# Kernel optimization log

Hardware: AMD Instinct MI355X
Metric: run time of the kernel (lower is better)

The kernel has to match this reference:

```python
import jax, jax.numpy as jnp
import numpy as np

B, S, D = 32, 1024, 512  # batch, seq_len, d_feat (= din = 2*dhid)

def setup_inputs() -> dict:
    key = jax.random.key(0)
    ks = jax.random.split(key, 8)
    x = jax.random.normal(ks[0], (B, S, D), dtype=jnp.float32)
    x_len = jax.random.randint(ks[1], (B,), 1, S + 1).astype(jnp.int32)
    w_score = jax.random.normal(ks[2], (D,), dtype=jnp.float32) * 0.02
    b_score = jnp.zeros((), dtype=jnp.float32)
    Wq = jax.random.normal(ks[3], (D, D), dtype=jnp.float32) * 0.02
    bq = jnp.zeros((D,), dtype=jnp.float32)
    Wk = jax.random.normal(ks[4], (D, D), dtype=jnp.float32) * 0.02
    bk = jnp.zeros((D,), dtype=jnp.float32)
    beta_raw = jax.random.uniform(ks[5], (1,), minval=-0.01, maxval=0.01, dtype=jnp.float32)
    return {"x": x, "x_len": x_len, "slot_idx": 0, "w_score": w_score, "b_score": b_score,
            "Wq": Wq, "bq": bq, "Wk": Wk, "bk": bk, "beta_raw": beta_raw}

def reference(x, x_len, slot_idx, w_score, b_score, Wq, bq, Wk, bk, beta_raw):
    # valid-position mask from per-sample lengths: [B, S]
    mask = jnp.arange(x.shape[1])[None, :] < x_len[:, None]
    neg_inf = jnp.float32(-jnp.inf)

    # ---- local branch: linear scorer -> masked softmax -> weighted sum ----
    local_scores = jnp.einsum('bsd,d->bs', x, w_score) + b_score          # [B, S]
    local_scores = jnp.where(mask, local_scores, neg_inf)
    local_w = jax.nn.softmax(local_scores, axis=1)
    c_local = jnp.einsum('bs,bsd->bd', local_w, x)                        # [B, D]

    # ---- global branch: QK bmm -> row-sum -> masked softmax -> weighted sum of x ----
    q = jnp.einsum('bsd,de->bse', x, Wq) + bq                             # [B, S, D]
    k = jnp.einsum('bsd,de->bse', x, Wk) + bk                             # [B, S, D]
    attn = jnp.einsum('bid,bjd->bij', q, k) / jnp.sqrt(jnp.float32(x.shape[2]))  # [B, S, S]
    g_scores = attn.sum(axis=2)                                           # [B, S] (sum over ALL j, as in source)
    g_scores = jnp.where(mask, g_scores, neg_inf)
    g_w = jax.nn.softmax(g_scores, axis=1)
    c_global = jnp.einsum('bs,bsd->bd', g_w, x)                           # [B, D]

    # ---- beta-weighted combination ----
    beta = jax.nn.sigmoid(beta_raw[slot_idx])
    c = c_local * beta + c_global * (1.0 - beta)
    return (x, c)
```

## Files before the change

kernel.cpp:

```cpp
#include <hip/hip_runtime.h>
#include <float.h>
#include <math.h>

#define BB 32
#define SS 1024
#define DD 512
#define NCH 32
#define CROWS 32
#define RW 8

typedef float f32x4 __attribute__((ext_vector_type(4)));

__device__ __forceinline__ float wave_reduce_add(float v) {
    #pragma unroll
    for (int m = 32; m >= 1; m >>= 1) v += __shfl_xor(v, m, 64);
    return v;
}

__global__ __launch_bounds__(256) void k_pass1(
    const float* __restrict__ x, const float* __restrict__ w_score,
    const int* __restrict__ x_len, float* __restrict__ out_x,
    float* __restrict__ xsum_part, float* __restrict__ lP,
    float* __restrict__ lm, float* __restrict__ lS)
{
    __shared__ float red_xsum[4][DD];
    __shared__ float red_ctx[4][DD];
    __shared__ float m_s[4], S_s[4];
    int b = blockIdx.x, sc = blockIdx.y;
    int wave = threadIdx.x >> 6, lane = threadIdx.x & 63, tid = threadIdx.x;
    int len = x_len[b];
    int s0 = sc * CROWS + wave * RW;
    size_t base = ((size_t)b * SS + s0) * DD;

    const f32x4* wr = (const f32x4*)w_score;
    f32x4 w0 = wr[lane], w1 = wr[lane + 64];

    f32x4 a[RW][2];
    #pragma unroll
    for (int r = 0; r < RW; ++r) {
        const f32x4* xr = (const f32x4*)(x + base + (size_t)r * DD);
        a[r][0] = xr[lane];
        a[r][1] = xr[lane + 64];
    }
    #pragma unroll
    for (int r = 0; r < RW; ++r) {
        f32x4* orow = (f32x4*)(out_x + base + (size_t)r * DD);
        __builtin_nontemporal_store(a[r][0], &orow[lane]);
        __builtin_nontemporal_store(a[r][1], &orow[lane + 64]);
    }
    float p[RW];
    f32x4 acc0 = {0,0,0,0}, acc1 = {0,0,0,0};
    #pragma unroll
    for (int r = 0; r < RW; ++r) {
        f32x4 t0 = a[r][0] * w0 + a[r][1] * w1;
        p[r] = t0.x + t0.y + t0.z + t0.w;
        acc0 += a[r][0];
        acc1 += a[r][1];
    }
    #pragma unroll
    for (int r = 0; r < RW; ++r) p[r] = wave_reduce_add(p[r]);
    float mw = -FLT_MAX;
    #pragma unroll
    for (int r = 0; r < RW; ++r) if (s0 + r < len) mw = fmaxf(mw, p[r]);
    float Sw = 0.f;
    f32x4 c0 = {0,0,0,0}, c1 = {0,0,0,0};
    #pragma unroll
    for (int r = 0; r < RW; ++r) {
        float wgt = (s0 + r < len) ? __expf(p[r] - mw) : 0.f;
        Sw += wgt;
        c0 += wgt * a[r][0];
        c1 += wgt * a[r][1];
    }
    f32x4* rx = (f32x4*)red_xsum[wave];
    f32x4* rc = (f32x4*)red_ctx[wave];
    rx[lane] = acc0; rx[lane + 64] = acc1;
    rc[lane] = c0;   rc[lane + 64] = c1;
    if (lane == 0) { m_s[wave] = mw; S_s[wave] = Sw; }
    __syncthreads();
    float mc = fmaxf(fmaxf(m_s[0], m_s[1]), fmaxf(m_s[2], m_s[3]));
    float e0 = __expf(m_s[0] - mc), e1 = __expf(m_s[1] - mc);
    float e2 = __expf(m_s[2] - mc), e3 = __expf(m_s[3] - mc);
    #pragma unroll
    for (int i = 0; i < 2; ++i) {
        int d = tid + i * 256;
        size_t off = ((size_t)b * NCH + sc) * DD + d;
        xsum_part[off] = red_xsum[0][d] + red_xsum[1][d] + red_xsum[2][d] + red_xsum[3][d];
        lP[off] = red_ctx[0][d]*e0 + red_ctx[1][d]*e1 + red_ctx[2][d]*e2 + red_ctx[3][d]*e3;
    }
    if (tid == 0) {
        lm[b * NCH + sc] = mc;
        lS[b * NCH + sc] = S_s[0]*e0 + S_s[1]*e1 + S_s[2]*e2 + S_s[3]*e3;
    }
}

__global__ __launch_bounds__(256) void k_ks(
    const float* __restrict__ xsum_part, const float* __restrict__ Wk,
    float* __restrict__ ks_part)
{
    __shared__ float xs[8][64];
    int dc = blockIdx.x, eb = blockIdx.y, bg = blockIdx.z;
    int tid = threadIdx.x;
    int e = eb * 256 + tid;
    #pragma unroll
    for (int k = 0; k < 2; ++k) {
        int i = tid + k * 256;
        int bi = i >> 6, dl = i & 63;
        int b = bg * 8 + bi, d = dc * 64 + dl;
        float v = 0.f;
        #pragma unroll 8
        for (int scc = 0; scc < NCH; ++scc)
            v += xsum_part[((size_t)b * NCH + scc) * DD + d];
        xs[bi][dl] = v;
    }
    __syncthreads();
    float acc[8] = {0,0,0,0,0,0,0,0};
    #pragma unroll 8
    for (int dl = 0; dl < 64; ++dl) {
        float w = Wk[(size_t)(dc * 64 + dl) * DD + e];
        #pragma unroll
        for (int bi = 0; bi < 8; ++bi) acc[bi] += xs[bi][dl] * w;
    }
    #pragma unroll
    for (int bi = 0; bi < 8; ++bi) {
        int b = bg * 8 + bi;
        ks_part[((size_t)dc * BB + b) * DD + e] = acc[bi];
    }
}

__global__ __launch_bounds__(256) void k_v(
    const float* __restrict__ ks_part, const float* __restrict__ Wq,
    const float* __restrict__ bk, float* __restrict__ v_part)
{
    __shared__ float wq_lds[256 * 65];
    __shared__ float ks_lds[8][64];
    int ec = blockIdx.x, db = blockIdx.y, bg = blockIdx.z;
    int tid = threadIdx.x;
    #pragma unroll
    for (int k = 0; k < 2; ++k) {
        int i = tid + k * 256;
        int bi = i >> 6, el = i & 63;
        int b = bg * 8 + bi, e = ec * 64 + el;
        float val = (float)SS * bk[e];
        #pragma unroll
        for (int dcc = 0; dcc < 8; ++dcc)
            val += ks_part[((size_t)dcc * BB + b) * DD + e];
        ks_lds[bi][el] = val;
    }
    #pragma unroll
    for (int it = 0; it < 16; ++it) {
        int idx = tid + it * 256;
        int rowd = idx >> 4, col4 = idx & 15;
        const f32x4 wv = *(const f32x4*)(Wq + (size_t)(db * 256 + rowd) * DD + ec * 64 + col4 * 4);
        float* dst = &wq_lds[rowd * 65 + col4 * 4];
        dst[0] = wv.x; dst[1] = wv.y; dst[2] = wv.z; dst[3] = wv.w;
    }
    __syncthreads();
    float acc[8] = {0,0,0,0,0,0,0,0};
    #pragma unroll 8
    for (int el = 0; el < 64; ++el) {
        float wq = wq_lds[tid * 65 + el];
        #pragma unroll
        for (int bi = 0; bi < 8; ++bi) acc[bi] += ks_lds[bi][el] * wq;
    }
    int d = db * 256 + tid;
    #pragma unroll
    for (int bi = 0; bi < 8; ++bi) {
        int b = bg * 8 + bi;
        v_part[((size_t)ec * BB + b) * DD + d] = acc[bi];
    }
}

__global__ __launch_bounds__(256) void k_pass2(
    const float* __restrict__ x, const float* __restrict__ v_part,
    const int* __restrict__ x_len,
    float* __restrict__ gP, float* __restrict__ gm, float* __restrict__ gS)
{
    __shared__ float v_lds[DD];
    __shared__ float red_ctx[4][DD];
    __shared__ float m_s[4], S_s[4];
    int b = blockIdx.x, sc = blockIdx.y;
    int wave = threadIdx.x >> 6, lane = threadIdx.x & 63, tid = threadIdx.x;
    int len = x_len[b];
    int s0 = sc * CROWS + wave * RW;
    size_t base = ((size_t)b * SS + s0) * DD;

    #pragma unroll
    for (int i = 0; i < 2; ++i) {
        int d = tid + i * 256;
        float vv = 0.f;
        #pragma unroll
        for (int ec = 0; ec < 8; ++ec) vv += v_part[((size_t)ec * BB + b) * DD + d];
        v_lds[d] = vv;
    }
    __syncthreads();
    const f32x4* vr = (const f32x4*)v_lds;
    f32x4 v0 = vr[lane], v1 = vr[lane + 64];

    f32x4 a[RW][2];
    #pragma unroll
    for (int r = 0; r < RW; ++r) {
        const f32x4* xr = (const f32x4*)(x + base + (size_t)r * DD);
        a[r][0] = xr[lane];
        a[r][1] = xr[lane + 64];
    }
    float p[RW];
    #pragma unroll
    for (int r = 0; r < RW; ++r) {
        f32x4 t0 = a[r][0] * v0 + a[r][1] * v1;
        p[r] = t0.x + t0.y + t0.z + t0.w;
    }
    #pragma unroll
    for (int r = 0; r < RW; ++r)
        p[r] = wave_reduce_add(p[r]) * 0.04419417382415922f;
    float mw = -FLT_MAX;
    #pragma unroll
    for (int r = 0; r < RW; ++r) if (s0 + r < len) mw = fmaxf(mw, p[r]);
    float Sw = 0.f;
    f32x4 c0 = {0,0,0,0}, c1 = {0,0,0,0};
    #pragma unroll
    for (int r = 0; r < RW; ++r) {
        float wgt = (s0 + r < len) ? __expf(p[r] - mw) : 0.f;
        Sw += wgt;
        c0 += wgt * a[r][0];
        c1 += wgt * a[r][1];
    }
    f32x4* rc = (f32x4*)red_ctx[wave];
    rc[lane] = c0; rc[lane + 64] = c1;
    if (lane == 0) { m_s[wave] = mw; S_s[wave] = Sw; }
    __syncthreads();
    float mc = fmaxf(fmaxf(m_s[0], m_s[1]), fmaxf(m_s[2], m_s[3]));
    float e0 = __expf(m_s[0] - mc), e1 = __expf(m_s[1] - mc);
    float e2 = __expf(m_s[2] - mc), e3 = __expf(m_s[3] - mc);
    #pragma unroll
    for (int i = 0; i < 2; ++i) {
        int d = tid + i * 256;
        size_t off = ((size_t)b * NCH + sc) * DD + d;
        gP[off] = red_ctx[0][d]*e0 + red_ctx[1][d]*e1 + red_ctx[2][d]*e2 + red_ctx[3][d]*e3;
    }
    if (tid == 0) {
        gm[b * NCH + sc] = mc;
        gS[b * NCH + sc] = S_s[0]*e0 + S_s[1]*e1 + S_s[2]*e2 + S_s[3]*e3;
    }
}

__global__ __launch_bounds__(512) void k_combine(
    const float* __restrict__ lP, const float* __restrict__ lm, const float* __restrict__ lS,
    const float* __restrict__ gP, const float* __restrict__ gm, const float* __restrict__ gS,
    const int* __restrict__ slot_idx, const float* __restrict__ beta_raw,
    float* __restrict__ out_c)
{
    int b = blockIdx.x, d = threadIdx.x;
    float Ml = -FLT_MAX, Mg = -FLT_MAX;
    #pragma unroll 8
    for (int c = 0; c < NCH; ++c) {
        Ml = fmaxf(Ml, lm[b * NCH + c]);
        Mg = fmaxf(Mg, gm[b * NCH + c]);
    }
    float Sl = 0.f, Pl = 0.f, Sg = 0.f, Pg = 0.f;
    #pragma unroll 4
    for (int c = 0; c < NCH; ++c) {
        float wl = __expf(lm[b * NCH + c] - Ml);
        float wg = __expf(gm[b * NCH + c] - Mg);
        Sl += lS[b * NCH + c] * wl;
        Sg += gS[b * NCH + c] * wg;
        Pl += lP[((size_t)b * NCH + c) * DD + d] * wl;
        Pg += gP[((size_t)b * NCH + c) * DD + d] * wg;
    }
    float br = beta_raw[slot_idx[0]];
    float beta = 1.f / (1.f + __expf(-br));
    out_c[b * DD + d] = beta * Pl / Sl + (1.f - beta) * Pg / Sg;
}

extern "C" void kernel_launch(void* const* d_in, const int* in_sizes, int n_in,
                              void* d_out, int out_size, void* d_ws, size_t ws_size,
                              hipStream_t stream) {
    const float* x        = (const float*)d_in[0];
    const int*   x_len    = (const int*)d_in[1];
    const int*   slot_idx = (const int*)d_in[2];
    const float* w_score  = (const float*)d_in[3];
    const float* Wq       = (const float*)d_in[5];
    const float* Wk       = (const float*)d_in[7];
    const float* bk       = (const float*)d_in[8];
    const float* beta_raw = (const float*)d_in[9];

    float* out   = (float*)d_out;
    float* out_x = out;
    float* out_c = out + (size_t)BB * SS * DD;

    float* ws = (float*)d_ws;
    float* ks_part   = ws;
    float* v_part    = ws + 131072;
    float* xsum_part = ws + 262144;
    float* lP        = ws + 786432;
    float* gP        = ws + 1310720;
    float* lm        = ws + 1835008;
    float* lS        = ws + 1836032;
    float* gm        = ws + 1837056;
    float* gS        = ws + 1838080;

    k_pass1<<<dim3(BB, NCH), 256, 0, stream>>>(x, w_score, x_len, out_x, xsum_part, lP, lm, lS);
    k_ks<<<dim3(8, 2, 4), 256, 0, stream>>>(xsum_part, Wk, ks_part);
    k_v<<<dim3(8, 2, 4), 256, 0, stream>>>(ks_part, Wq, bk, v_part);
    k_pass2<<<dim3(BB, NCH), 256, 0, stream>>>(x, v_part, x_len, gP, gm, gS);
    k_combine<<<BB, 512, 0, stream>>>(lP, lm, lS, gP, gm, gS, slot_idx, beta_raw, out_c);
}
```

Baseline: 58.53 us.

## Fuse ks/v matvecs into one kernel and fold combine into pass2 via last-block atomic

The two small matvec kernels (xsum·Wk, then ks·Wq) become a single per-batch kernel that recomputes ks redundantly in each of its two blocks, removing the partial-sum buffers. The final combine kernel is folded into pass2: each block bumps a per-batch atomic counter, and the last block for that batch does the cross-chunk softmax merge and writes the output. This cuts two kernel launches and their partial-buffer traffic. In exchange it adds a memset launch, much lower parallelism in the matvec kernel (64 blocks, each streaming all of Wk), and threadfence/atomic synchronisation overhead.

```diff
diff --git a/kernel.cpp b/kernel.cpp
--- a/kernel.cpp
+++ b/kernel.cpp
@@ -93,105 +93,74 @@
     }
 }
 
-__global__ __launch_bounds__(256) void k_ks(
+__global__ __launch_bounds__(256) void k_v2(
     const float* __restrict__ xsum_part, const float* __restrict__ Wk,
-    float* __restrict__ ks_part)
+    const float* __restrict__ Wq, const float* __restrict__ bk,
+    float* __restrict__ v)
 {
-    __shared__ float xs[8][64];
-    int dc = blockIdx.x, eb = blockIdx.y, bg = blockIdx.z;
-    int tid = threadIdx.x;
-    int e = eb * 256 + tid;
-    #pragma unroll
-    for (int k = 0; k < 2; ++k) {
-        int i = tid + k * 256;
-        int bi = i >> 6, dl = i & 63;
-        int b = bg * 8 + bi, d = dc * 64 + dl;
-        float v = 0.f;
+    __shared__ float xs[DD];
+    __shared__ float ks[DD];
+    __shared__ float tile[256][65];
+    int dh = blockIdx.x, b = blockIdx.y, tid = threadIdx.x;
+    #pragma unroll
+    for (int i = 0; i < 2; ++i) {
+        int d = tid + i * 256;
+        float s = 0.f;
         #pragma unroll 8
-        for (int scc = 0; scc < NCH; ++scc)
-            v += xsum_part[((size_t)b * NCH + scc) * DD + d];
-        xs[bi][dl] = v;
-    }
-    __syncthreads();
-    float acc[8] = {0,0,0,0,0,0,0,0};
+        for (int sc = 0; sc < NCH; ++sc)
+            s += xsum_part[((size_t)b * NCH + sc) * DD + d];
+        xs[d] = s;
+    }
+    __syncthreads();
+    float k0 = (float)SS * bk[tid], k1 = (float)SS * bk[tid + 256];
     #pragma unroll 8
-    for (int dl = 0; dl < 64; ++dl) {
-        float w = Wk[(size_t)(dc * 64 + dl) * DD + e];
+    for (int d = 0; d < DD; ++d) {
+        float xv = xs[d];
+        k0 += xv * Wk[(size_t)d * DD + tid];
+        k1 += xv * Wk[(size_t)d * DD + tid + 256];
+    }
+    ks[tid] = k0; ks[tid + 256] = k1;
+    __syncthreads();
+    int d0 = dh * 256;
+    float acc = 0.f;
+    for (int ec = 0; ec < 8; ++ec) {
         #pragma unroll
-        for (int bi = 0; bi < 8; ++bi) acc[bi] += xs[bi][dl] * w;
-    }
-    #pragma unroll
-    for (int bi = 0; bi < 8; ++bi) {
-        int b = bg * 8 + bi;
-        ks_part[((size_t)dc * BB + b) * DD + e] = acc[bi];
-    }
-}
-
-__global__ __launch_bounds__(256) void k_v(
-    const float* __restrict__ ks_part, const float* __restrict__ Wq,
-    const float* __restrict__ bk, float* __restrict__ v_part)
-{
-    __shared__ float wq_lds[256 * 65];
-    __shared__ float ks_lds[8][64];
-    int ec = blockIdx.x, db = blockIdx.y, bg = blockIdx.z;
-    int tid = threadIdx.x;
-    #pragma unroll
-    for (int k = 0; k < 2; ++k) {
-        int i = tid + k * 256;
-        int bi = i >> 6, el = i & 63;
-        int b = bg * 8 + bi, e = ec * 64 + el;
-        float val = (float)SS * bk[e];
-        #pragma unroll
-        for (int dcc = 0; dcc < 8; ++dcc)
-            val += ks_part[((size_t)dcc * BB + b) * DD + e];
-        ks_lds[bi][el] = val;
-    }
-    #pragma unroll
-    for (int it = 0; it < 16; ++it) {
-        int idx = tid + it * 256;
-        int rowd = idx >> 4, col4 = idx & 15;
-        const f32x4 wv = *(const f32x4*)(Wq + (size_t)(db * 256 + rowd) * DD + ec * 64 + col4 * 4);
-        float* dst = &wq_lds[rowd * 65 + col4 * 4];
-        dst[0] = wv.x; dst[1] = wv.y; dst[2] = wv.z; dst[3] = wv.w;
-    }
-    __syncthreads();
-    float acc[8] = {0,0,0,0,0,0,0,0};
-    #pragma unroll 8
-    for (int el = 0; el < 64; ++el) {
-        float wq = wq_lds[tid * 65 + el];
-        #pragma unroll
-        for (int bi = 0; bi < 8; ++bi) acc[bi] += ks_lds[bi][el] * wq;
-    }
-    int d = db * 256 + tid;
-    #pragma unroll
-    for (int bi = 0; bi < 8; ++bi) {
-        int b = bg * 8 + bi;
-        v_part[((size_t)ec * BB + b) * DD + d] = acc[bi];
-    }
+        for (int it = 0; it < 16; ++it) {
+            int idx = tid + it * 256;
+            int rowd = idx >> 4, col4 = idx & 15;
+            f32x4 wv = *(const f32x4*)(Wq + (size_t)(d0 + rowd) * DD + ec * 64 + col4 * 4);
+            float* dst = &tile[rowd][col4 * 4];
+            dst[0] = wv.x; dst[1] = wv.y; dst[2] = wv.z; dst[3] = wv.w;
+        }
+        __syncthreads();
+        #pragma unroll 8
+        for (int el = 0; el < 64; ++el)
+            acc += tile[tid][el] * ks[ec * 64 + el];
+        __syncthreads();
+    }
+    v[(size_t)b * DD + d0 + tid] = acc;
 }
 
 __global__ __launch_bounds__(256) void k_pass2(
-    const float* __restrict__ x, const float* __restrict__ v_part,
+    const float* __restrict__ x, const float* __restrict__ v,
     const int* __restrict__ x_len,
-    float* __restrict__ gP, float* __restrict__ gm, float* __restrict__ gS)
+    const float* __restrict__ lP, const float* __restrict__ lm, const float* __restrict__ lS,
+    float* __restrict__ gP, float* __restrict__ gm, float* __restrict__ gS,
+    int* __restrict__ cnt, const int* __restrict__ slot_idx,
+    const float* __restrict__ beta_raw, float* __restrict__ out_c)
 {
     __shared__ float v_lds[DD];
     __shared__ float red_ctx[4][DD];
     __shared__ float m_s[4], S_s[4];
+    __shared__ int lastflag;
     int b = blockIdx.x, sc = blockIdx.y;
     int wave = threadIdx.x >> 6, lane = threadIdx.x & 63, tid = threadIdx.x;
     int len = x_len[b];
     int s0 = sc * CROWS + wave * RW;
     size_t base = ((size_t)b * SS + s0) * DD;
 
-    #pragma unroll
-    for (int i = 0; i < 2; ++i) {
-        int d = tid + i * 256;
-        float vv = 0.f;
-        #pragma unroll
-        for (int ec = 0; ec < 8; ++ec) vv += v_part[((size_t)ec * BB + b) * DD + d];
-        v_lds[d] = vv;
-    }
+    v_lds[tid] = v[(size_t)b * DD + tid];
+    v_lds[tid + 256] = v[(size_t)b * DD + tid + 256];
     __syncthreads();
     const f32x4* vr = (const f32x4*)v_lds;
     f32x4 v0 = vr[lane], v1 = vr[lane + 64];
@@ -241,34 +210,40 @@
         gm[b * NCH + sc] = mc;
         gS[b * NCH + sc] = S_s[0]*e0 + S_s[1]*e1 + S_s[2]*e2 + S_s[3]*e3;
     }
-}
-
-__global__ __launch_bounds__(512) void k_combine(
-    const float* __restrict__ lP, const float* __restrict__ lm, const float* __restrict__ lS,
-    const float* __restrict__ gP, const float* __restrict__ gm, const float* __restrict__ gS,
-    const int* __restrict__ slot_idx, const float* __restrict__ beta_raw,
-    float* __restrict__ out_c)
-{
-    int b = blockIdx.x, d = threadIdx.x;
+    __threadfence();
+    if (tid == 0) {
+        int old = atomicAdd(&cnt[b], 1);
+        lastflag = (old == NCH - 1);
+    }
+    __syncthreads();
+    if (!lastflag) return;
+    __threadfence();
+
     float Ml = -FLT_MAX, Mg = -FLT_MAX;
     #pragma unroll 8
     for (int c = 0; c < NCH; ++c) {
         Ml = fmaxf(Ml, lm[b * NCH + c]);
         Mg = fmaxf(Mg, gm[b * NCH + c]);
     }
-    float Sl = 0.f, Pl = 0.f, Sg = 0.f, Pg = 0.f;
+    float Sl = 0.f, Sg = 0.f;
+    float Pl0 = 0.f, Pl1 = 0.f, Pg0 = 0.f, Pg1 = 0.f;
     #pragma unroll 4
     for (int c = 0; c < NCH; ++c) {
         float wl = __expf(lm[b * NCH + c] - Ml);
         float wg = __expf(gm[b * NCH + c] - Mg);
         Sl += lS[b * NCH + c] * wl;
         Sg += gS[b * NCH + c] * wg;
-        Pl += lP[((size_t)b * NCH + c) * DD + d] * wl;
-        Pg += gP[((size_t)b * NCH + c) * DD + d] * wg;
+        size_t off = ((size_t)b * NCH + c) * DD + tid;
+        Pl0 += lP[off] * wl;
+        Pl1 += lP[off + 256] * wl;
+        Pg0 += gP[off] * wg;
+        Pg1 += gP[off + 256] * wg;
     }
     float br = beta_raw[slot_idx[0]];
     float beta = 1.f / (1.f + __expf(-br));
-    out_c[b * DD + d] = beta * Pl / Sl + (1.f - beta) * Pg / Sg;
+    float rb = 1.f - beta;
+    out_c[(size_t)b * DD + tid]       = beta * Pl0 / Sl + rb * Pg0 / Sg;
+    out_c[(size_t)b * DD + tid + 256] = beta * Pl1 / Sl + rb * Pg1 / Sg;
 }
 
 extern "C" void kernel_launch(void* const* d_in, const int* in_sizes, int n_in,
@@ -288,19 +263,19 @@
     float* out_c = out + (size_t)BB * SS * DD;
 
     float* ws = (float*)d_ws;
-    float* ks_part   = ws;
-    float* v_part    = ws + 131072;
-    float* xsum_part = ws + 262144;
-    float* lP        = ws + 786432;
-    float* gP        = ws + 1310720;
-    float* lm        = ws + 1835008;
-    float* lS        = ws + 1836032;
-    float* gm        = ws + 1837056;
-    float* gS        = ws + 1838080;
-
+    float* xsum_part = ws;
+    float* lP        = ws + 524288;
+    float* gP        = ws + 1048576;
+    float* v         = ws + 1572864;
+    float* lm        = ws + 1589248;
+    float* lS        = ws + 1590272;
+    float* gm        = ws + 1591296;
+    float* gS        = ws + 1592320;
+    int*   cnt       = (int*)(ws + 1593344);
+
+    hipMemsetAsync(cnt, 0, BB * sizeof(int), stream);
     k_pass1<<<dim3(BB, NCH), 256, 0, stream>>>(x, w_score, x_len, out_x, xsum_part, lP, lm, lS);
-    k_ks<<<dim3(8, 2, 4), 256, 0, stream>>>(xsum_part, Wk, ks_part);
-    k_v<<<dim3(8, 2, 4), 256, 0, stream>>>(ks_part, Wq, bk, v_part);
-    k_pass2<<<dim3(BB, NCH), 256, 0, stream>>>(x, v_part, x_len, gP, gm, gS);
-    k_combine<<<BB, 512, 0, stream>>>(lP, lm, lS, gP, gm, gS, slot_idx, beta_raw, out_c);
-}
+    k_v2<<<dim3(2, BB), 256, 0, stream>>>(xsum_part, Wk, Wq, bk, v);
+    k_pass2<<<dim3(BB, NCH), 256, 0, stream>>>(x, v, x_len, lP, lm, lS, gP, gm, gS,
+                                               cnt, slot_idx, beta_raw, out_c);
+}
```

After: 212.4 us. 263% more time.

## Split x column-sum into its own pass and fuse local and global softmax passes

Applied to the files above, without the earlier changes.

Moves the x row-sum into a dedicated lightweight read-only kernel so the projection chain can start without waiting on the out_x copy. The local and global scoring passes are merged into one kernel that reads x once and computes both weighted sums. The out_x copy moves to this last pass. Total x traffic stays about the same, and the separate sum kernel uses narrow 2-wide loads with limited parallelism, which may underuse bandwidth.

```diff
diff --git a/kernel.cpp b/kernel.cpp
--- a/kernel.cpp
+++ b/kernel.cpp
@@ -8,8 +8,10 @@
 #define NCH 32
 #define CROWS 32
 #define RW 8
+#define NXCH 16
 
 typedef float f32x4 __attribute__((ext_vector_type(4)));
+typedef float f32x2 __attribute__((ext_vector_type(2)));
 
 __device__ __forceinline__ float wave_reduce_add(float v) {
     #pragma unroll
@@ -17,21 +19,123 @@
     return v;
 }
 
-__global__ __launch_bounds__(256) void k_pass1(
+__global__ __launch_bounds__(256) void k_xsumx(
+    const float* __restrict__ x, float* __restrict__ xsum_part)
+{
+    int sc = blockIdx.x, b = blockIdx.y, tid = threadIdx.x;
+    const float* xb = x + ((size_t)b * SS + sc * 64) * DD + tid * 2;
+    f32x2 acc = {0.f, 0.f};
+    #pragma unroll 8
+    for (int r = 0; r < 64; ++r)
+        acc += *(const f32x2*)(xb + (size_t)r * DD);
+    *(f32x2*)(xsum_part + ((size_t)b * NXCH + sc) * DD + tid * 2) = acc;
+}
+
+__global__ __launch_bounds__(256) void k_ks(
+    const float* __restrict__ xsum_part, const float* __restrict__ Wk,
+    float* __restrict__ ks_part)
+{
+    __shared__ float xs[8][64];
+    int dc = blockIdx.x, eb = blockIdx.y, bg = blockIdx.z;
+    int tid = threadIdx.x;
+    int e = eb * 256 + tid;
+    #pragma unroll
+    for (int k = 0; k < 2; ++k) {
+        int i = tid + k * 256;
+        int bi = i >> 6, dl = i & 63;
+        int b = bg * 8 + bi, d = dc * 64 + dl;
+        float v = 0.f;
+        #pragma unroll
+        for (int scc = 0; scc < NXCH; ++scc)
+            v += xsum_part[((size_t)b * NXCH + scc) * DD + d];
+        xs[bi][dl] = v;
+    }
+    __syncthreads();
+    float acc[8] = {0,0,0,0,0,0,0,0};
+    #pragma unroll 8
+    for (int dl = 0; dl < 64; ++dl) {
+        float w = Wk[(size_t)(dc * 64 + dl) * DD + e];
+        #pragma unroll
+        for (int bi = 0; bi < 8; ++bi) acc[bi] += xs[bi][dl] * w;
+    }
+    #pragma unroll
+    for (int bi = 0; bi < 8; ++bi) {
+        int b = bg * 8 + bi;
+        ks_part[((size_t)dc * BB + b) * DD + e] = acc[bi];
+    }
+}
+
+__global__ __launch_bounds__(256) void k_v(
+    const float* __restrict__ ks_part, const float* __restrict__ Wq,
+    const float* __restrict__ bk, float* __restrict__ v_part)
+{
+    __shared__ float wq_lds[256 * 65];
+    __shared__ float ks_lds[8][64];
+    int ec = blockIdx.x, db = blockIdx.y, bg = blockIdx.z;
+    int tid = threadIdx.x;
+    #pragma unroll
+    for (int k = 0; k < 2; ++k) {
+        int i = tid + k * 256;
+        int bi = i >> 6, el = i & 63;
+        int b = bg * 8 + bi, e = ec * 64 + el;
+        float val = (float)SS * bk[e];
+        #pragma unroll
+        for (int dcc = 0; dcc < 8; ++dcc)
+            val += ks_part[((size_t)dcc * BB + b) * DD + e];
+        ks_lds[bi][el] = val;
+    }
+    #pragma unroll
+    for (int it = 0; it < 16; ++it) {
+        int idx = tid + it * 256;
+        int rowd = idx >> 4, col4 = idx & 15;
+        f32x4 wv = *(const f32x4*)(Wq + (size_t)(db * 256 + rowd) * DD + ec * 64 + col4 * 4);
+        float* dst = &wq_lds[rowd * 65 + col4 * 4];
+        dst[0] = wv.x; dst[1] = wv.y; dst[2] = wv.z; dst[3] = wv.w;
+    }
+    __syncthreads();
+    float acc[8] = {0,0,0,0,0,0,0,0};
+    #pragma unroll 8
+    for (int el = 0; el < 64; ++el) {
+        float wq = wq_lds[tid * 65 + el];
+        #pragma unroll
+        for (int bi = 0; bi < 8; ++bi) acc[bi] += ks_lds[bi][el] * wq;
+    }
+    int d = db * 256 + tid;
+    #pragma unroll
+    for (int bi = 0; bi < 8; ++bi) {
+        int b = bg * 8 + bi;
+        v_part[((size_t)ec * BB + b) * DD + d] = acc[bi];
+    }
+}
+
+__global__ __launch_bounds__(256) void k_pass1full(
     const float* __restrict__ x, const float* __restrict__ w_score,
-    const int* __restrict__ x_len, float* __restrict__ out_x,
-    float* __restrict__ xsum_part, float* __restrict__ lP,
-    float* __restrict__ lm, float* __restrict__ lS)
-{
-    __shared__ float red_xsum[4][DD];
-    __shared__ float red_ctx[4][DD];
-    __shared__ float m_s[4], S_s[4];
+    const float* __restrict__ v_part, const int* __restrict__ x_len,
+    float* __restrict__ out_x,
+    float* __restrict__ lP, float* __restrict__ lm, float* __restrict__ lS,
+    float* __restrict__ gP, float* __restrict__ gm, float* __restrict__ gS)
+{
+    __shared__ float v_lds[DD];
+    __shared__ float red_l[4][DD];
+    __shared__ float red_g[4][DD];
+    __shared__ float msl[4], Ssl[4], msg[4], Ssg[4];
     int b = blockIdx.x, sc = blockIdx.y;
     int wave = threadIdx.x >> 6, lane = threadIdx.x & 63, tid = threadIdx.x;
     int len = x_len[b];
     int s0 = sc * CROWS + wave * RW;
     size_t base = ((size_t)b * SS + s0) * DD;
 
+    #pragma unroll
+    for (int i = 0; i < 2; ++i) {
+        int d = tid + i * 256;
+        float vv = 0.f;
+        #pragma unroll
+        for (int ec = 0; ec < 8; ++ec) vv += v_part[((size_t)ec * BB + b) * DD + d];
+        v_lds[d] = vv;
+    }
+    __syncthreads();
+    const f32x4* vr = (const f32x4*)v_lds;
+    f32x4 v0 = vr[lane], v1 = vr[lane + 64];
     const f32x4* wr = (const f32x4*)w_score;
     f32x4 w0 = wr[lane], w1 = wr[lane + 64];
 
@@ -48,198 +152,62 @@
         __builtin_nontemporal_store(a[r][0], &orow[lane]);
         __builtin_nontemporal_store(a[r][1], &orow[lane + 64]);
     }
-    float p[RW];
-    f32x4 acc0 = {0,0,0,0}, acc1 = {0,0,0,0};
+    float pl[RW], pg[RW];
     #pragma unroll
     for (int r = 0; r < RW; ++r) {
         f32x4 t0 = a[r][0] * w0 + a[r][1] * w1;
-        p[r] = t0.x + t0.y + t0.z + t0.w;
-        acc0 += a[r][0];
-        acc1 += a[r][1];
-    }
-    #pragma unroll
-    for (int r = 0; r < RW; ++r) p[r] = wave_reduce_add(p[r]);
-    float mw = -FLT_MAX;
-    #pragma unroll
-    for (int r = 0; r < RW; ++r) if (s0 + r < len) mw = fmaxf(mw, p[r]);
-    float Sw = 0.f;
-    f32x4 c0 = {0,0,0,0}, c1 = {0,0,0,0};
-    #pragma unroll
-    for (int r = 0; r < RW; ++r) {
-        float wgt = (s0 + r < len) ? __expf(p[r] - mw) : 0.f;
-        Sw += wgt;
-        c0 += wgt * a[r][0];
-        c1 += wgt * a[r][1];
-    }
-    f32x4* rx = (f32x4*)red_xsum[wave];
-    f32x4* rc = (f32x4*)red_ctx[wave];
-    rx[lane] = acc0; rx[lane + 64] = acc1;
-    rc[lane] = c0;   rc[lane + 64] = c1;
-    if (lane == 0) { m_s[wave] = mw; S_s[wave] = Sw; }
-    __syncthreads();
-    float mc = fmaxf(fmaxf(m_s[0], m_s[1]), fmaxf(m_s[2], m_s[3]));
-    float e0 = __expf(m_s[0] - mc), e1 = __expf(m_s[1] - mc);
-    float e2 = __expf(m_s[2] - mc), e3 = __expf(m_s[3] - mc);
+        pl[r] = t0.x + t0.y + t0.z + t0.w;
+        f32x4 u0 = a[r][0] * v0 + a[r][1] * v1;
+        pg[r] = u0.x + u0.y + u0.z + u0.w;
+    }
+    #pragma unroll
+    for (int r = 0; r < RW; ++r) {
+        pl[r] = wave_reduce_add(pl[r]);
+        pg[r] = wave_reduce_add(pg[r]) * 0.04419417382415922f;
+    }
+    float mwl = -FLT_MAX, mwg = -FLT_MAX;
+    #pragma unroll
+    for (int r = 0; r < RW; ++r) {
+        if (s0 + r < len) {
+            mwl = fmaxf(mwl, pl[r]);
+            mwg = fmaxf(mwg, pg[r]);
+        }
+    }
+    float Swl = 0.f, Swg = 0.f;
+    f32x4 cl0 = {0,0,0,0}, cl1 = {0,0,0,0}, cg0 = {0,0,0,0}, cg1 = {0,0,0,0};
+    #pragma unroll
+    for (int r = 0; r < RW; ++r) {
+        bool valid = (s0 + r) < len;
+        float wl = valid ? __expf(pl[r] - mwl) : 0.f;
+        float wg = valid ? __expf(pg[r] - mwg) : 0.f;
+        Swl += wl; Swg += wg;
+        cl0 += wl * a[r][0]; cl1 += wl * a[r][1];
+        cg0 += wg * a[r][0]; cg1 += wg * a[r][1];
+    }
+    f32x4* rl = (f32x4*)red_l[wave];
+    f32x4* rg = (f32x4*)red_g[wave];
+    rl[lane] = cl0; rl[lane + 64] = cl1;
+    rg[lane] = cg0; rg[lane + 64] = cg1;
+    if (lane == 0) { msl[wave] = mwl; Ssl[wave] = Swl; msg[wave] = mwg; Ssg[wave] = Swg; }
+    __syncthreads();
+    float mcl = fmaxf(fmaxf(msl[0], msl[1]), fmaxf(msl[2], msl[3]));
+    float mcg = fmaxf(fmaxf(msg[0], msg[1]), fmaxf(msg[2], msg[3]));
+    float el0 = __expf(msl[0] - mcl), el1 = __expf(msl[1] - mcl);
+    float el2 = __expf(msl[2] - mcl), el3 = __expf(msl[3] - mcl);
+    float eg0 = __expf(msg[0] - mcg), eg1 = __expf(msg[1] - mcg);
+    float eg2 = __expf(msg[2] - mcg), eg3 = __expf(msg[3] - mcg);
     #pragma unroll
     for (int i = 0; i < 2; ++i) {
         int d = tid + i * 256;
         size_t off = ((size_t)b * NCH + sc) * DD + d;
-        xsum_part[off] = red_xsum[0][d] + red_xsum[1][d] + red_xsum[2][d] + red_xsum[3][d];
-        lP[off] = red_ctx[0][d]*e0 + red_ctx[1][d]*e1 + red_ctx[2][d]*e2 + red_ctx[3][d]*e3;
+        lP[off] = red_l[0][d]*el0 + red_l[1][d]*el1 + red_l[2][d]*el2 + red_l[3][d]*el3;
+        gP[off] = red_g[0][d]*eg0 + red_g[1][d]*eg1 + red_g[2][d]*eg2 + red_g[3][d]*eg3;
     }
     if (tid == 0) {
-        lm[b * NCH + sc] = mc;
-        lS[b * NCH + sc] = S_s[0]*e0 + S_s[1]*e1 + S_s[2]*e2 + S_s[3]*e3;
-    }
-}
-
-__global__ __launch_bounds__(256) void k_ks(
-    const float* __restrict__ xsum_part, const float* __restrict__ Wk,
-    float* __restrict__ ks_part)
-{
-    __shared__ float xs[8][64];
-    int dc = blockIdx.x, eb = blockIdx.y, bg = blockIdx.z;
-    int tid = threadIdx.x;
-    int e = eb * 256 + tid;
-    #pragma unroll
-    for (int k = 0; k < 2; ++k) {
-        int i = tid + k * 256;
-        int bi = i >> 6, dl = i & 63;
-        int b = bg * 8 + bi, d = dc * 64 + dl;
-        float v = 0.f;
-        #pragma unroll 8
-        for (int scc = 0; scc < NCH; ++scc)
-            v += xsum_part[((size_t)b * NCH + scc) * DD + d];
-        xs[bi][dl] = v;
-    }
-    __syncthreads();
-    float acc[8] = {0,0,0,0,0,0,0,0};
-    #pragma unroll 8
-    for (int dl = 0; dl < 64; ++dl) {
-        float w = Wk[(size_t)(dc * 64 + dl) * DD + e];
-        #pragma unroll
-        for (int bi = 0; bi < 8; ++bi) acc[bi] += xs[bi][dl] * w;
-    }
-    #pragma unroll
-    for (int bi = 0; bi < 8; ++bi) {
-        int b = bg * 8 + bi;
-        ks_part[((size_t)dc * BB + b) * DD + e] = acc[bi];
-    }
-}
-
-__global__ __launch_bounds__(256) void k_v(
-    const float* __restrict__ ks_part, const float* __restrict__ Wq,
-    const float* __restrict__ bk, float* __restrict__ v_part)
-{
-    __shared__ float wq_lds[256 * 65];
-    __shared__ float ks_lds[8][64];
-    int ec = blockIdx.x, db = blockIdx.y, bg = blockIdx.z;
-    int tid = threadIdx.x;
-    #pragma unroll
-    for (int k = 0; k < 2; ++k) {
-        int i = tid + k * 256;
-        int bi = i >> 6, el = i & 63;
-        int b = bg * 8 + bi, e = ec * 64 + el;
-        float val = (float)SS * bk[e];
-        #pragma unroll
-        for (int dcc = 0; dcc < 8; ++dcc)
-            val += ks_part[((size_t)dcc * BB + b) * DD + e];
-        ks_lds[bi][el] = val;
-    }
-    #pragma unroll
-    for (int it = 0; it < 16; ++it) {
-        int idx = tid + it * 256;
-        int rowd = idx >> 4, col4 = idx & 15;
-        const f32x4 wv = *(const f32x4*)(Wq + (size_t)(db * 256 + rowd) * DD + ec * 64 + col4 * 4);
-        float* dst = &wq_lds[rowd * 65 + col4 * 4];
-        dst[0] = wv.x; dst[1] = wv.y; dst[2] = wv.z; dst[3] = wv.w;
-    }
-    __syncthreads();
-    float acc[8] = {0,0,0,0,0,0,0,0};
-    #pragma unroll 8
-    for (int el = 0; el < 64; ++el) {
-        float wq = wq_lds[tid * 65 + el];
-        #pragma unroll
-        for (int bi = 0; bi < 8; ++bi) acc[bi] += ks_lds[bi][el] * wq;
-    }
-    int d = db * 256 + tid;
-    #pragma unroll
-    for (int bi = 0; bi < 8; ++bi) {
-        int b = bg * 8 + bi;
-        v_part[((size_t)ec * BB + b) * DD + d] = acc[bi];
-    }
-}
-
-__global__ __launch_bounds__(256) void k_pass2(
-    const float* __restrict__ x, const float* __restrict__ v_part,
-    const int* __restrict__ x_len,
-    float* __restrict__ gP, float* __restrict__ gm, float* __restrict__ gS)
-{
-    __shared__ float v_lds[DD];
-    __shared__ float red_ctx[4][DD];
-    __shared__ float m_s[4], S_s[4];
-    int b = blockIdx.x, sc = blockIdx.y;
-    int wave = threadIdx.x >> 6, lane = threadIdx.x & 63, tid = threadIdx.x;
-    int len = x_len[b];
-    int s0 = sc * CROWS + wave * RW;
-    size_t base = ((size_t)b * SS + s0) * DD;
-
-    #pragma unroll
-    for (int i = 0; i < 2; ++i) {
-        int d = tid + i * 256;
-        float vv = 0.f;
-        #pragma unroll
-        for (int ec = 0; ec < 8; ++ec) vv += v_part[((size_t)ec * BB + b) * DD + d];
-        v_lds[d] = vv;
-    }
-    __syncthreads();
-    const f32x4* vr = (const f32x4*)v_lds;
-    f32x4 v0 = vr[lane], v1 = vr[lane + 64];
-
-    f32x4 a[RW][2];
-    #pragma unroll
-    for (int r = 0; r < RW; ++r) {
-        const f32x4* xr = (const f32x4*)(x + base + (size_t)r * DD);
-        a[r][0] = xr[lane];
-        a[r][1] = xr[lane + 64];
-    }
-    float p[RW];
-    #pragma unroll
-    for (int r = 0; r < RW; ++r) {
-        f32x4 t0 = a[r][0] * v0 + a[r][1] * v1;
-        p[r] = t0.x + t0.y + t0.z + t0.w;
-    }
-    #pragma unroll
-    for (int r = 0; r < RW; ++r)
-        p[r] = wave_reduce_add(p[r]) * 0.04419417382415922f;
-    float mw = -FLT_MAX;
-    #pragma unroll
-    for (int r = 0; r < RW; ++r) if (s0 + r < len) mw = fmaxf(mw, p[r]);
-    float Sw = 0.f;
-    f32x4 c0 = {0,0,0,0}, c1 = {0,0,0,0};
-    #pragma unroll
-    for (int r = 0; r < RW; ++r) {
-        float wgt = (s0 + r < len) ? __expf(p[r] - mw) : 0.f;
-        Sw += wgt;
-        c0 += wgt * a[r][0];
-        c1 += wgt * a[r][1];
-    }
-    f32x4* rc = (f32x4*)red_ctx[wave];
-    rc[lane] = c0; rc[lane + 64] = c1;
-    if (lane == 0) { m_s[wave] = mw; S_s[wave] = Sw; }
-    __syncthreads();
-    float mc = fmaxf(fmaxf(m_s[0], m_s[1]), fmaxf(m_s[2], m_s[3]));
-    float e0 = __expf(m_s[0] - mc), e1 = __expf(m_s[1] - mc);
-    float e2 = __expf(m_s[2] - mc), e3 = __expf(m_s[3] - mc);
-    #pragma unroll
-    for (int i = 0; i < 2; ++i) {
-        int d = tid + i * 256;
-        size_t off = ((size_t)b * NCH + sc) * DD + d;
-        gP[off] = red_ctx[0][d]*e0 + red_ctx[1][d]*e1 + red_ctx[2][d]*e2 + red_ctx[3][d]*e3;
-    }
-    if (tid == 0) {
-        gm[b * NCH + sc] = mc;
-        gS[b * NCH + sc] = S_s[0]*e0 + S_s[1]*e1 + S_s[2]*e2 + S_s[3]*e3;
+        lm[b * NCH + sc] = mcl;
+        lS[b * NCH + sc] = Ssl[0]*el0 + Ssl[1]*el1 + Ssl[2]*el2 + Ssl[3]*el3;
+        gm[b * NCH + sc] = mcg;
+        gS[b * NCH + sc] = Ssg[0]*eg0 + Ssg[1]*eg1 + Ssg[2]*eg2 + Ssg[3]*eg3;
     }
 }
 
@@ -288,19 +256,20 @@
     float* out_c = out + (size_t)BB * SS * DD;
 
     float* ws = (float*)d_ws;
-    float* ks_part   = ws;
-    float* v_part    = ws + 131072;
-    float* xsum_part = ws + 262144;
-    float* lP        = ws + 786432;
-    float* gP        = ws + 1310720;
-    float* lm        = ws + 1835008;
-    float* lS        = ws + 1836032;
-    float* gm        = ws + 1837056;
-    float* gS        = ws + 1838080;
-
-    k_pass1<<<dim3(BB, NCH), 256, 0, stream>>>(x, w_score, x_len, out_x, xsum_part, lP, lm, lS);
+    float* xsum_part = ws;
+    float* ks_part   = ws + 262144;
+    float* v_part    = ws + 393216;
+    float* lP        = ws + 524288;
+    float* gP        = ws + 1048576;
+    float* lm        = ws + 1572864;
+    float* lS        = ws + 1573888;
+    float* gm        = ws + 1574912;
+    float* gS        = ws + 1575936;
+
+    k_xsumx<<<dim3(NXCH, BB), 256, 0, stream>>>(x, xsum_part);
     k_ks<<<dim3(8, 2, 4), 256, 0, stream>>>(xsum_part, Wk, ks_part);
     k_v<<<dim3(8, 2, 4), 256, 0, stream>>>(ks_part, Wq, bk, v_part);
-    k_pass2<<<dim3(BB, NCH), 256, 0, stream>>>(x, v_part, x_len, gP, gm, gS);
+    k_pass1full<<<dim3(BB, NCH), 256, 0, stream>>>(x, w_score, v_part, x_len, out_x,
+                                                   lP, lm, lS, gP, gm, gS);
     k_combine<<<BB, 512, 0, stream>>>(lP, lm, lS, gP, gm, gS, slot_idx, beta_raw, out_c);
 }
```

Result: no change. 57.49 us (median of 2 runs) (-1.8%).

## Give each wave its own 16-row chunk with online softmax, dropping LDS reductions

Applied to the files above, without the earlier changes.

The two streaming passes move from block-level work, where four waves each took 8 rows and were merged through shared memory with a barrier, to independent waves. Each wave handles a 16-row chunk in two groups of 8 and keeps an online-softmax running max, sum and context. This removes LDS traffic and __syncthreads and reads v_part straight into registers. The cost is twice as many partial chunks (64 per batch), which enlarges the workspace and the partial-result traffic seen by k_ks and k_combine, and there are half as many blocks (512).

```diff
diff --git a/kernel.cpp b/kernel.cpp
--- a/kernel.cpp
+++ b/kernel.cpp
@@ -5,8 +5,8 @@
 #define BB 32
 #define SS 1024
 #define DD 512
-#define NCH 32
-#define CROWS 32
+#define NCH 64
+#define CHR 16
 #define RW 8
 
 typedef float f32x4 __attribute__((ext_vector_type(4)));
@@ -17,80 +17,73 @@
     return v;
 }
 
-__global__ __launch_bounds__(256) void k_pass1(
+__global__ __launch_bounds__(256) void k_p1(
     const float* __restrict__ x, const float* __restrict__ w_score,
     const int* __restrict__ x_len, float* __restrict__ out_x,
     float* __restrict__ xsum_part, float* __restrict__ lP,
     float* __restrict__ lm, float* __restrict__ lS)
 {
-    __shared__ float red_xsum[4][DD];
-    __shared__ float red_ctx[4][DD];
-    __shared__ float m_s[4], S_s[4];
-    int b = blockIdx.x, sc = blockIdx.y;
-    int wave = threadIdx.x >> 6, lane = threadIdx.x & 63, tid = threadIdx.x;
+    int wave = threadIdx.x >> 6, lane = threadIdx.x & 63;
+    int wid = blockIdx.x * 4 + wave;
+    int b = wid >> 6, ch = wid & 63;
     int len = x_len[b];
-    int s0 = sc * CROWS + wave * RW;
-    size_t base = ((size_t)b * SS + s0) * DD;
+    int s0 = ch * CHR;
 
     const f32x4* wr = (const f32x4*)w_score;
     f32x4 w0 = wr[lane], w1 = wr[lane + 64];
 
-    f32x4 a[RW][2];
-    #pragma unroll
-    for (int r = 0; r < RW; ++r) {
-        const f32x4* xr = (const f32x4*)(x + base + (size_t)r * DD);
-        a[r][0] = xr[lane];
-        a[r][1] = xr[lane + 64];
-    }
-    #pragma unroll
-    for (int r = 0; r < RW; ++r) {
-        f32x4* orow = (f32x4*)(out_x + base + (size_t)r * DD);
-        __builtin_nontemporal_store(a[r][0], &orow[lane]);
-        __builtin_nontemporal_store(a[r][1], &orow[lane + 64]);
-    }
-    float p[RW];
-    f32x4 acc0 = {0,0,0,0}, acc1 = {0,0,0,0};
-    #pragma unroll
-    for (int r = 0; r < RW; ++r) {
-        f32x4 t0 = a[r][0] * w0 + a[r][1] * w1;
-        p[r] = t0.x + t0.y + t0.z + t0.w;
-        acc0 += a[r][0];
-        acc1 += a[r][1];
-    }
-    #pragma unroll
-    for (int r = 0; r < RW; ++r) p[r] = wave_reduce_add(p[r]);
-    float mw = -FLT_MAX;
-    #pragma unroll
-    for (int r = 0; r < RW; ++r) if (s0 + r < len) mw = fmaxf(mw, p[r]);
-    float Sw = 0.f;
+    f32x4 xa0 = {0,0,0,0}, xa1 = {0,0,0,0};
     f32x4 c0 = {0,0,0,0}, c1 = {0,0,0,0};
-    #pragma unroll
-    for (int r = 0; r < RW; ++r) {
-        float wgt = (s0 + r < len) ? __expf(p[r] - mw) : 0.f;
-        Sw += wgt;
-        c0 += wgt * a[r][0];
-        c1 += wgt * a[r][1];
-    }
-    f32x4* rx = (f32x4*)red_xsum[wave];
-    f32x4* rc = (f32x4*)red_ctx[wave];
-    rx[lane] = acc0; rx[lane + 64] = acc1;
-    rc[lane] = c0;   rc[lane + 64] = c1;
-    if (lane == 0) { m_s[wave] = mw; S_s[wave] = Sw; }
-    __syncthreads();
-    float mc = fmaxf(fmaxf(m_s[0], m_s[1]), fmaxf(m_s[2], m_s[3]));
-    float e0 = __expf(m_s[0] - mc), e1 = __expf(m_s[1] - mc);
-    float e2 = __expf(m_s[2] - mc), e3 = __expf(m_s[3] - mc);
-    #pragma unroll
-    for (int i = 0; i < 2; ++i) {
-        int d = tid + i * 256;
-        size_t off = ((size_t)b * NCH + sc) * DD + d;
-        xsum_part[off] = red_xsum[0][d] + red_xsum[1][d] + red_xsum[2][d] + red_xsum[3][d];
-        lP[off] = red_ctx[0][d]*e0 + red_ctx[1][d]*e1 + red_ctx[2][d]*e2 + red_ctx[3][d]*e3;
-    }
-    if (tid == 0) {
-        lm[b * NCH + sc] = mc;
-        lS[b * NCH + sc] = S_s[0]*e0 + S_s[1]*e1 + S_s[2]*e2 + S_s[3]*e3;
-    }
+    float m = -FLT_MAX, S = 0.f;
+
+    for (int g = 0; g < CHR / RW; ++g) {
+        int sg = s0 + g * RW;
+        size_t base = ((size_t)b * SS + sg) * DD;
+        f32x4 a[RW][2];
+        #pragma unroll
+        for (int r = 0; r < RW; ++r) {
+            const f32x4* xr = (const f32x4*)(x + base + (size_t)r * DD);
+            a[r][0] = xr[lane];
+            a[r][1] = xr[lane + 64];
+        }
+        #pragma unroll
+        for (int r = 0; r < RW; ++r) {
+            f32x4* orow = (f32x4*)(out_x + base + (size_t)r * DD);
+            __builtin_nontemporal_store(a[r][0], &orow[lane]);
+            __builtin_nontemporal_store(a[r][1], &orow[lane + 64]);
+        }
+        float p[RW];
+        #pragma unroll
+        for (int r = 0; r < RW; ++r) {
+            f32x4 t = a[r][0] * w0 + a[r][1] * w1;
+            p[r] = t.x + t.y + t.z + t.w;
+            xa0 += a[r][0];
+            xa1 += a[r][1];
+        }
+        #pragma unroll
+        for (int r = 0; r < RW; ++r) p[r] = wave_reduce_add(p[r]);
+        float gmax = -FLT_MAX;
+        #pragma unroll
+        for (int r = 0; r < RW; ++r) if (sg + r < len) gmax = fmaxf(gmax, p[r]);
+        float nm = fmaxf(m, gmax);
+        float sc = __expf(m - nm);
+        S *= sc; c0 *= sc; c1 *= sc;
+        #pragma unroll
+        for (int r = 0; r < RW; ++r) {
+            bool valid = (sg + r) < len;
+            float wgt = valid ? __expf(p[r] - nm) : 0.f;
+            S += wgt;
+            c0 += wgt * a[r][0];
+            c1 += wgt * a[r][1];
+        }
+        m = nm;
+    }
+    size_t off = ((size_t)b * NCH + ch) * DD + lane * 4;
+    *(f32x4*)(xsum_part + off)       = xa0;
+    *(f32x4*)(xsum_part + off + 256) = xa1;
+    *(f32x4*)(lP + off)       = c0;
+    *(f32x4*)(lP + off + 256) = c1;
+    if (lane == 0) { lm[b * NCH + ch] = m; lS[b * NCH + ch] = S; }
 }
 
 __global__ __launch_bounds__(256) void k_ks(
@@ -150,7 +143,7 @@
     for (int it = 0; it < 16; ++it) {
         int idx = tid + it * 256;
         int rowd = idx >> 4, col4 = idx & 15;
-        const f32x4 wv = *(const f32x4*)(Wq + (size_t)(db * 256 + rowd) * DD + ec * 64 + col4 * 4);
+        f32x4 wv = *(const f32x4*)(Wq + (size_t)(db * 256 + rowd) * DD + ec * 64 + col4 * 4);
         float* dst = &wq_lds[rowd * 65 + col4 * 4];
         dst[0] = wv.x; dst[1] = wv.y; dst[2] = wv.z; dst[3] = wv.w;
     }
@@ -170,77 +163,67 @@
     }
 }
 
-__global__ __launch_bounds__(256) void k_pass2(
+__global__ __launch_bounds__(256) void k_p2(
     const float* __restrict__ x, const float* __restrict__ v_part,
     const int* __restrict__ x_len,
     float* __restrict__ gP, float* __restrict__ gm, float* __restrict__ gS)
 {
-    __shared__ float v_lds[DD];
-    __shared__ float red_ctx[4][DD];
-    __shared__ float m_s[4], S_s[4];
-    int b = blockIdx.x, sc = blockIdx.y;
-    int wave = threadIdx.x >> 6, lane = threadIdx.x & 63, tid = threadIdx.x;
+    int wave = threadIdx.x >> 6, lane = threadIdx.x & 63;
+    int wid = blockIdx.x * 4 + wave;
+    int b = wid >> 6, ch = wid & 63;
     int len = x_len[b];
-    int s0 = sc * CROWS + wave * RW;
-    size_t base = ((size_t)b * SS + s0) * DD;
-
-    #pragma unroll
-    for (int i = 0; i < 2; ++i) {
-        int d = tid + i * 256;
-        float vv = 0.f;
-        #pragma unroll
-        for (int ec = 0; ec < 8; ++ec) vv += v_part[((size_t)ec * BB + b) * DD + d];
-        v_lds[d] = vv;
-    }
-    __syncthreads();
-    const f32x4* vr = (const f32x4*)v_lds;
-    f32x4 v0 = vr[lane], v1 = vr[lane + 64];
-
-    f32x4 a[RW][2];
-    #pragma unroll
-    for (int r = 0; r < RW; ++r) {
-        const f32x4* xr = (const f32x4*)(x + base + (size_t)r * DD);
-        a[r][0] = xr[lane];
-        a[r][1] = xr[lane + 64];
-    }
-    float p[RW];
-    #pragma unroll
-    for (int r = 0; r < RW; ++r) {
-        f32x4 t0 = a[r][0] * v0 + a[r][1] * v1;
-        p[r] = t0.x + t0.y + t0.z + t0.w;
-    }
-    #pragma unroll
-    for (int r = 0; r < RW; ++r)
-        p[r] = wave_reduce_add(p[r]) * 0.04419417382415922f;
-    float mw = -FLT_MAX;
-    #pragma unroll
-    for (int r = 0; r < RW; ++r) if (s0 + r < len) mw = fmaxf(mw, p[r]);
-    float Sw = 0.f;
+    int s0 = ch * CHR;
+
+    f32x4 v0 = {0,0,0,0}, v1 = {0,0,0,0};
+    #pragma unroll
+    for (int ec = 0; ec < 8; ++ec) {
+        const f32x4* vp = (const f32x4*)(v_part + ((size_t)ec * BB + b) * DD);
+        v0 += vp[lane];
+        v1 += vp[lane + 64];
+    }
+
     f32x4 c0 = {0,0,0,0}, c1 = {0,0,0,0};
-    #pragma unroll
-    for (int r = 0; r < RW; ++r) {
-        float wgt = (s0 + r < len) ? __expf(p[r] - mw) : 0.f;
-        Sw += wgt;
-        c0 += wgt * a[r][0];
-        c1 += wgt * a[r][1];
-    }
-    f32x4* rc = (f32x4*)red_ctx[wave];
-    rc[lane] = c0; rc[lane + 64] = c1;
-    if (lane == 0) { m_s[wave] = mw; S_s[wave] = Sw; }
-    __syncthreads();
-    float mc = fmaxf(fmaxf(m_s[0], m_s[1]), fmaxf(m_s[2], m_s[3]));
-    float e0 = __expf(m_s[0] - mc), e1 = __expf(m_s[1] - mc);
-    float e2 = __expf(m_s[2] - mc), e3 = __expf(m_s[3] - mc);
-    #pragma unroll
-    for (int i = 0; i < 2; ++i) {
-        int d = tid + i * 256;
-        size_t off = ((size_t)b * NCH + sc) * DD + d;
-        gP[off] = red_ctx[0][d]*e0 + red_ctx[1][d]*e1 + red_ctx[2][d]*e2 + red_ctx[3][d]*e3;
-    }
-    if (tid == 0) {
-        gm[b * NCH + sc] = mc;
-        gS[b * NCH + sc] = S_s[0]*e0 + S_s[1]*e1 + S_s[2]*e2 + S_s[3]*e3;
-    }
+    float m = -FLT_MAX, S = 0.f;
+
+    for (int g = 0; g < CHR / RW; ++g) {
+        int sg = s0 + g * RW;
+        size_t base = ((size_t)b * SS + sg) * DD;
+        f32x4 a[RW][2];
+        #pragma unroll
+        for (int r = 0; r < RW; ++r) {
+            const f32x4* xr = (const f32x4*)(x + base + (size_t)r * DD);
+            a[r][0] = xr[lane];
+            a[r][1] = xr[lane + 64];
+        }
+        float p[RW];
+        #pragma unroll
+        for (int r = 0; r < RW; ++r) {
+            f32x4 t = a[r][0] * v0 + a[r][1] * v1;
+            p[r] = t.x + t.y + t.z + t.w;
+        }
+        #pragma unroll
+        for (int r = 0; r < RW; ++r)
+            p[r] = wave_reduce_add(p[r]) * 0.04419417382415922f;
+        float gmax = -FLT_MAX;
+        #pragma unroll
+        for (int r = 0; r < RW; ++r) if (sg + r < len) gmax = fmaxf(gmax, p[r]);
+        float nm = fmaxf(m, gmax);
+        float sc = __expf(m - nm);
+        S *= sc; c0 *= sc; c1 *= sc;
+        #pragma unroll
+        for (int r = 0; r < RW; ++r) {
+            bool valid = (sg + r) < len;
+            float wgt = valid ? __expf(p[r] - nm) : 0.f;
+            S += wgt;
+            c0 += wgt * a[r][0];
+            c1 += wgt * a[r][1];
+        }
+        m = nm;
+    }
+    size_t off = ((size_t)b * NCH + ch) * DD + lane * 4;
+    *(f32x4*)(gP + off)       = c0;
+    *(f32x4*)(gP + off + 256) = c1;
+    if (lane == 0) { gm[b * NCH + ch] = m; gS[b * NCH + ch] = S; }
 }
 
 __global__ __launch_bounds__(512) void k_combine(
@@ -288,19 +271,19 @@
     float* out_c = out + (size_t)BB * SS * DD;
 
     float* ws = (float*)d_ws;
-    float* ks_part   = ws;
-    float* v_part    = ws + 131072;
-    float* xsum_part = ws + 262144;
-    float* lP        = ws + 786432;
-    float* gP        = ws + 1310720;
-    float* lm        = ws + 1835008;
-    float* lS        = ws + 1836032;
-    float* gm        = ws + 1837056;
-    float* gS        = ws + 1838080;
-
-    k_pass1<<<dim3(BB, NCH), 256, 0, stream>>>(x, w_score, x_len, out_x, xsum_part, lP, lm, lS);
+    float* xsum_part = ws;
+    float* lP        = ws + 1048576;
+    float* gP        = ws + 2097152;
+    float* ks_part   = ws + 3145728;
+    float* v_part    = ws + 3276800;
+    float* lm        = ws + 3407872;
+    float* lS        = ws + 3409920;
+    float* gm        = ws + 3411968;
+    float* gS        = ws + 3414016;
+
+    k_p1<<<512, 256, 0, stream>>>(x, w_score, x_len, out_x, xsum_part, lP, lm, lS);
     k_ks<<<dim3(8, 2, 4), 256, 0, stream>>>(xsum_part, Wk, ks_part);
     k_v<<<dim3(8, 2, 4), 256, 0, stream>>>(ks_part, Wq, bk, v_part);
-    k_pass2<<<dim3(BB, NCH), 256, 0, stream>>>(x, v_part, x_len, gP, gm, gS);
+    k_p2<<<512, 256, 0, stream>>>(x, v_part, x_len, gP, gm, gS);
     k_combine<<<BB, 512, 0, stream>>>(lP, lm, lS, gP, gm, gS, slot_idx, beta_raw, out_c);
 }
```

New measurement: 66.19 us. 13.1% more time.
